# Optimization experiments

Measured on AMD Instinct MI355X. Metric: run time of the kernel, lower is better.

Reference implementation:

```python
import jax, jax.numpy as jnp
import numpy as np

HEADS = 16
LN_EPS = 1e-5


def setup_inputs() -> dict:
    key = jax.random.key(0)
    ks = jax.random.split(key, 8)
    B, S, D = 2, 2048, 1024
    F = 4 * D
    std = 0.02
    return {
        "x": jax.random.normal(ks[0], (B, S, D), jnp.float32),
        # QKV projections (stored as (in, out)); kaiming-normal-like scale
        "Wq": jax.random.normal(ks[1], (D, D), jnp.float32) * std,
        "bq": jnp.zeros((D,), jnp.float32),
        "Wk": jax.random.normal(ks[2], (D, D), jnp.float32) * std,
        "bk": jnp.zeros((D,), jnp.float32),
        "Wv": jax.random.normal(ks[3], (D, D), jnp.float32) * std,
        "bv": jnp.zeros((D,), jnp.float32),
        # FFN
        "W1": jax.random.normal(ks[4], (D, F), jnp.float32) * std,
        "b1": jnp.zeros((F,), jnp.float32),
        "W2": jax.random.normal(ks[5], (F, D), jnp.float32) * std,
        "b2": jnp.zeros((D,), jnp.float32),
        # LayerNorm
        "gamma": jnp.ones((D,), jnp.float32),
        "beta": jnp.zeros((D,), jnp.float32),
    }


def reference(x, Wq, bq, Wk, bk, Wv, bv, W1, b1, W2, b2, gamma, beta):
    B, S, D = x.shape
    H = HEADS
    hd = D // H
    # QKV projections -> [B, H, S, hd]
    Q = (x @ Wq + bq).reshape(B, S, H, hd).transpose(0, 2, 1, 3)
    K = (x @ Wk + bk).reshape(B, S, H, hd).transpose(0, 2, 1, 3)
    V = (x @ Wv + bv).reshape(B, S, H, hd).transpose(0, 2, 1, 3)
    # scores scaled by sqrt(embedding_dim), faithful to source (not head_dim)
    scores = jnp.einsum('bhqd,bhkd->bhqk', Q, K) / jnp.sqrt(jnp.asarray(D, x.dtype))
    attn = jax.nn.softmax(scores, axis=-1)
    # diagonal_training: zero the diagonal of the post-softmax attention matrix
    attn = attn * (1.0 - jnp.eye(S, dtype=attn.dtype))
    out = jnp.einsum('bhqk,bhkd->bhqd', attn, V)
    out = out.transpose(0, 2, 1, 3).reshape(B, S, D)
    # dropout is identity in eval mode
    h = jax.nn.gelu(out @ W1 + b1, approximate=False) @ W2 + b2
    # LayerNorm
    mu = jnp.mean(h, axis=-1, keepdims=True)
    var = jnp.var(h, axis=-1, keepdims=True)
    return (h - mu) * jax.lax.rsqrt(var + LN_EPS) * gamma + beta
```

## Files before the change

### kernel.cpp

```cpp
#include <hip/hip_runtime.h>

using bf16x8 = __attribute__((ext_vector_type(8))) short;
using f32x4  = __attribute__((ext_vector_type(4))) float;

__device__ __forceinline__ float b2f(ushort u) {
  union { unsigned int i; float f; } v; v.i = ((unsigned int)u) << 16; return v.f;
}
__device__ __forceinline__ ushort f2b(float f) {
  unsigned int x = __float_as_uint(f);
  unsigned int r = (x + 0x7FFFu + ((x >> 16) & 1u)) >> 16;
  return (ushort)r;
}
__device__ __forceinline__ unsigned cvt_pk_bf16(float a, float b) {
  unsigned r;
  asm("v_cvt_pk_bf16_f32 %0, %1, %2" : "=v"(r) : "v"(a), "v"(b));
  return r;
}

__device__ __forceinline__ void gld_lds16(const void* g, void* l) {
  __builtin_amdgcn_global_load_lds(
      (const __attribute__((address_space(1))) void*)g,
      (__attribute__((address_space(3))) void*)l, 16, 0, 0);
}


__global__ void cast_bf16_kernel(const float* __restrict__ in, ushort* __restrict__ out, int n) {
  int i = (blockIdx.x * blockDim.x + threadIdx.x) * 4;
  if (i < n) {
    float4 v = *(const float4*)(in + i);
    ushort4 o = make_ushort4(f2b(v.x), f2b(v.y), f2b(v.z), f2b(v.w));
    *(ushort4*)(out + i) = o;
  }
}

__global__ void transpose_cast_kernel(const float* __restrict__ in, ushort* __restrict__ out,
                                      int R, int C) {
  __shared__ float tile[32][33];
  int tx = threadIdx.x, ty = threadIdx.y;
  int cb = blockIdx.x * 32, rb = blockIdx.y * 32;
  for (int i = ty; i < 32; i += 8)
    tile[i][tx] = in[(size_t)(rb + i) * C + (cb + tx)];
  __syncthreads();
  for (int i = ty; i < 32; i += 8)
    out[(size_t)(cb + i) * R + (rb + tx)] = f2b(tile[tx][i]);
}

__global__ void transpose_cast_qkv_kernel(const float* __restrict__ Wq,
                                          const float* __restrict__ Wk,
                                          const float* __restrict__ Wv,
                                          ushort* __restrict__ out) {
  __shared__ float tile[32][33];
  const float* in = (blockIdx.z == 0) ? Wq : (blockIdx.z == 1) ? Wk : Wv;
  ushort* dst = out + (size_t)blockIdx.z * 1024 * 1024;
  int tx = threadIdx.x, ty = threadIdx.y;
  int cb = blockIdx.x * 32, rb = blockIdx.y * 32;
  for (int i = ty; i < 32; i += 8)
    tile[i][tx] = in[(size_t)(rb + i) * 1024 + (cb + tx)];
  __syncthreads();
  for (int i = ty; i < 32; i += 8)
    dst[(size_t)(cb + i) * 1024 + (rb + tx)] = f2b(tile[tx][i]);
}

__global__ void transpose_v_kernel(const ushort* __restrict__ V, ushort* __restrict__ Vt) {
  __shared__ ushort t[32][33];
  int bh = blockIdx.z;
  int b = bh >> 4, h = bh & 15;
  int s0 = blockIdx.x * 32, d0 = blockIdx.y * 32;
  const ushort* Vbp = V + ((size_t)b * 2048) * 1024 + h * 64;
  ushort* Vtb = Vt + (size_t)bh * 64 * 2048;
  int tx = threadIdx.x, ty = threadIdx.y;
  for (int i = ty; i < 32; i += 8) t[i][tx] = Vbp[(size_t)(s0 + i) * 1024 + d0 + tx];
  __syncthreads();
  for (int i = ty; i < 32; i += 8) Vtb[(size_t)(d0 + i) * 2048 + s0 + tx] = t[tx][i];
}


template<int EPI>
__global__ __launch_bounds__(512) void gemm256(
    const ushort* __restrict__ A, const ushort* __restrict__ Bt,
    const float* __restrict__ bias, void* __restrict__ Cout,
    int M, int N, int K)
{
  extern __shared__ ushort lds[];

  const int nwg = gridDim.x * gridDim.y;
  const int bid = blockIdx.y * gridDim.x + blockIdx.x;
  const int cpx = nwg >> 3;
  const int swz = (bid & 7) * cpx + (bid >> 3);
  const int bm = (swz % gridDim.x) * 256;
  const int bn = (swz / gridDim.x) * 256;

  const int tid = threadIdx.x;
  const int lane = tid & 63, w = tid >> 6;
  const int wr = w >> 2, wc = w & 3;
  const int hi = lane >> 4, c = lane & 15;

  const int srow0 = tid >> 3;
  const int scolx = (((tid & 7) ^ (srow0 & 7)) * 8);
  const ushort* gA = A  + (size_t)(bm + srow0) * K + scolx;
  const ushort* gB = Bt + (size_t)(bn + srow0) * K + scolx;

  const int NT = K / 64;
  f32x4 acc[8][4] = {};

  auto STAGE = [&](int buf, int t) {
    ushort* bA = lds + buf * 32768;
    ushort* bB = bA + 16384;
    const size_t ko = (size_t)t * 64;
    #pragma unroll
    for (int ch = 0; ch < 4; ++ch) {
      gld_lds16(gA + (size_t)ch * 64 * K + ko, bA + ch * 4096 + tid * 8);
      gld_lds16(gB + (size_t)ch * 64 * K + ko, bB + ch * 4096 + tid * 8);
    }
  };

  STAGE(0, 0);
  __syncthreads();

  int cur = 0;
  for (int t = 0; t < NT; ++t) {
    if (t + 1 < NT) STAGE(cur ^ 1, t + 1);
    const ushort* sA = lds + cur * 32768;
    const ushort* sB = sA + 16384;
    #pragma unroll
    for (int kk = 0; kk < 2; ++kk) {
      bf16x8 bf[4], af[8];
      #pragma unroll
      for (int n = 0; n < 4; ++n) {
        int row = wc * 64 + n * 16 + c;
        bf[n] = *(const bf16x8*)&sB[row * 64 + (((kk * 4 + hi) ^ (c & 7)) * 8)];
      }
      #pragma unroll
      for (int m = 0; m < 8; ++m) {
        int row = wr * 128 + m * 16 + c;
        af[m] = *(const bf16x8*)&sA[row * 64 + (((kk * 4 + hi) ^ (c & 7)) * 8)];
      }
      __builtin_amdgcn_s_setprio(1);
      #pragma unroll
      for (int m = 0; m < 8; ++m)
        #pragma unroll
        for (int n = 0; n < 4; ++n)
          acc[m][n] = __builtin_amdgcn_mfma_f32_16x16x32_bf16(af[m], bf[n], acc[m][n], 0, 0, 0);
      __builtin_amdgcn_s_setprio(0);
    }
    __syncthreads();
    cur ^= 1;
  }

  ushort* eb = &lds[w * 1088];
  const int g = hi;
  const int er = lane >> 3;
  const int es = (lane & 7) * 8;
  float bia[4];
  #pragma unroll
  for (int n = 0; n < 4; ++n) bia[n] = bias[bn + wc * 64 + n * 16 + c];

  #pragma unroll
  for (int mf = 0; mf < 8; ++mf) {
    #pragma unroll
    for (int n = 0; n < 4; ++n) {
      #pragma unroll
      for (int r = 0; r < 4; ++r) {
        float v = acc[mf][n][r] + bia[n];
        if (EPI == 1) {
          float u = 0.7978845608028654f * (v + 0.044715f * v * v * v);
          float au = fabsf(u);
          float e = __expf(-2.0f * au);
          float th = (1.0f - e) / (1.0f + e);
          th = copysignf(th, u);
          v = 0.5f * v * (1.0f + th);
        }
        eb[(g * 4 + r) * 68 + n * 16 + c] = f2b(v);
      }
    }
    asm volatile("" ::: "memory");
    bf16x8 v0 = *(const bf16x8*)&eb[er * 68 + es];
    bf16x8 v1 = *(const bf16x8*)&eb[(er + 8) * 68 + es];
    int grow = bm + wr * 128 + mf * 16 + er;
    int gcol = bn + wc * 64 + es;
    if (EPI == 3) {
      ushort* dst = (ushort*)Cout + (size_t)(gcol >> 10) * 4194304 + (gcol & 1023);
      *(bf16x8*)(dst + (size_t)grow * 1024) = v0;
      *(bf16x8*)(dst + (size_t)(grow + 8) * 1024) = v1;
    } else {
      ushort* dst = (ushort*)Cout + gcol;
      *(bf16x8*)(dst + (size_t)grow * N) = v0;
      *(bf16x8*)(dst + (size_t)(grow + 8) * N) = v1;
    }
    asm volatile("" ::: "memory");
  }
}


#define BM 128
#define BN 128
#define BK 32

__global__ __launch_bounds__(256) void gemm_bf16_f32(
    const ushort* __restrict__ A, const ushort* __restrict__ Bt,
    float* __restrict__ C0, float* __restrict__ C1,
    float* __restrict__ C2, float* __restrict__ C3,
    int M, int N, int Kstride, int k_len)
{
  __shared__ ushort Asm_[2][BM * BK];
  __shared__ ushort Bsm_[2][BN * BK];
  const int bm = blockIdx.x * BM, bn = blockIdx.y * BN;
  const int k_begin = blockIdx.z * k_len;
  const int tid = threadIdx.x;
  const int lane = tid & 63, w = tid >> 6;
  const int wm = (w >> 1) * 64, wn = (w & 1) * 64;
  const int g = lane >> 4, c = lane & 15;
  const int swz8 = ((g ^ ((c >> 1) & 3)) * 8);
  const int srow = tid >> 2;
  const int scol = (((tid & 3) ^ ((srow >> 1) & 3)) * 8);
  const int soff = srow * 32 + (tid & 3) * 8;

  const ushort* gA0 = A  + (size_t)(bm + srow) * Kstride + k_begin + scol;
  const ushort* gA1 = gA0 + (size_t)64 * Kstride;
  const ushort* gB0 = Bt + (size_t)(bn + srow) * Kstride + k_begin + scol;
  const ushort* gB1 = gB0 + (size_t)64 * Kstride;

  f32x4 acc[4][4] = {};
  const int nt = k_len / BK;

  gld_lds16(gA0, &Asm_[0][soff]);
  gld_lds16(gA1, &Asm_[0][64 * 32 + soff]);
  gld_lds16(gB0, &Bsm_[0][soff]);
  gld_lds16(gB1, &Bsm_[0][64 * 32 + soff]);
  __syncthreads();

  int cur = 0;
  for (int t = 0; t < nt; ++t) {
    if (t + 1 < nt) {
      int k0 = (t + 1) * BK;
      gld_lds16(gA0 + k0, &Asm_[cur ^ 1][soff]);
      gld_lds16(gA1 + k0, &Asm_[cur ^ 1][64 * 32 + soff]);
      gld_lds16(gB0 + k0, &Bsm_[cur ^ 1][soff]);
      gld_lds16(gB1 + k0, &Bsm_[cur ^ 1][64 * 32 + soff]);
    }
    bf16x8 af[4], bfr[4];
    #pragma unroll
    for (int m = 0; m < 4; ++m)
      af[m] = *(const bf16x8*)&Asm_[cur][(wm + m * 16 + c) * 32 + swz8];
    #pragma unroll
    for (int n = 0; n < 4; ++n)
      bfr[n] = *(const bf16x8*)&Bsm_[cur][(wn + n * 16 + c) * 32 + swz8];
    #pragma unroll
    for (int m = 0; m < 4; ++m)
      #pragma unroll
      for (int n = 0; n < 4; ++n)
        acc[m][n] = __builtin_amdgcn_mfma_f32_16x16x32_bf16(af[m], bfr[n], acc[m][n], 0, 0, 0);
    __syncthreads();
    cur ^= 1;
  }

  float* dst = C0;
  if (blockIdx.z == 1) dst = C1;
  else if (blockIdx.z == 2) dst = C2;
  else if (blockIdx.z == 3) dst = C3;

  #pragma unroll
  for (int n = 0; n < 4; ++n) {
    int col = bn + wn + n * 16 + c;
    #pragma unroll
    for (int m = 0; m < 4; ++m)
      #pragma unroll
      for (int r = 0; r < 4; ++r) {
        int row = bm + wm + m * 16 + g * 4 + r;
        dst[(size_t)row * N + col] = acc[m][n][r];
      }
  }
}


#define ATT_SC2 0.0450842202f

__global__ __launch_bounds__(512) void attn_kernel(
    const ushort* __restrict__ Q, const ushort* __restrict__ K,
    const ushort* __restrict__ V, const ushort* __restrict__ Vt,
    ushort* __restrict__ Out)
{
  const int bid = blockIdx.x;
  const int tile = (bid & 7) * 64 + (bid >> 3);
  const int bh = tile >> 4;
  const int q0 = (tile & 15) * 128;
  const int b = bh >> 4, h = bh & 15;
  const int tid = threadIdx.x;
  const int w = tid >> 6, lane = tid & 63;
  const int hi = lane >> 4, c = lane & 15;
  const int qw = q0 + w * 16;

  const size_t boff = ((size_t)b * 2048) * 1024 + h * 64;
  const ushort* Qp = Q + boff;
  const ushort* Kp = K + boff;
  const ushort* Vp = V + boff;
  const ushort* Vtb = Vt + (size_t)bh * 64 * 2048;

  __shared__ ushort Ksm[2][64 * 64];
  __shared__ ushort Vsm[2][64 * 64];
  __shared__ ushort Psm[8][16 * 72];

  const int srow = tid >> 3;
  const int sslot = tid & 7;
  const int scolx = ((sslot ^ (srow & 7)) * 8);
  const ushort* gK = Kp + (size_t)srow * 1024 + scolx;
  const ushort* gV = Vtb + (size_t)srow * 2048 + scolx;

  bf16x8 qf0 = *(const bf16x8*)(Qp + (size_t)(qw + c) * 1024 + hi * 8);
  bf16x8 qf1 = *(const bf16x8*)(Qp + (size_t)(qw + c) * 1024 + 32 + hi * 8);
  {
    ushort* q0p = (ushort*)&qf0;
    ushort* q1p = (ushort*)&qf1;
    #pragma unroll
    for (int j = 0; j < 8; ++j) {
      q0p[j] = f2b(b2f(q0p[j]) * ATT_SC2);
      q1p[j] = f2b(b2f(q1p[j]) * ATT_SC2);
    }
  }

  f32x4 acc[4] = {};
  float l_run = 0.f;

  gld_lds16(gK, &Ksm[0][tid * 8]);
  gld_lds16(gV, &Vsm[0][tid * 8]);
  __syncthreads();

  const int nt = 2048 / 64;
  for (int t = 0; t < nt; ++t) {
    const int buf = t & 1;
    if (t + 1 < nt) {
      gld_lds16(gK + (size_t)(t + 1) * 64 * 1024, &Ksm[buf ^ 1][tid * 8]);
      gld_lds16(gV + (size_t)(t + 1) * 64,        &Vsm[buf ^ 1][tid * 8]);
    }

    f32x4 sv[4];
    __builtin_amdgcn_s_setprio(1);
    #pragma unroll
    for (int sub = 0; sub < 4; ++sub) {
      int rr = sub * 16 + c;
      int sw = (rr & 7) * 8;
      bf16x8 k0 = *(const bf16x8*)&Ksm[buf][rr * 64 + ((hi * 8) ^ sw)];
      bf16x8 k1 = *(const bf16x8*)&Ksm[buf][rr * 64 + ((32 + hi * 8) ^ sw)];
      f32x4 z = {};
      z = __builtin_amdgcn_mfma_f32_16x16x32_bf16(k0, qf0, z, 0, 0, 0);
      z = __builtin_amdgcn_mfma_f32_16x16x32_bf16(k1, qf1, z, 0, 0, 0);
      sv[sub] = z;
    }
    __builtin_amdgcn_s_setprio(0);

    float p[16];
    float psum = 0.f;
    #pragma unroll
    for (int sub = 0; sub < 4; ++sub)
      #pragma unroll
      for (int r = 0; r < 4; ++r) { float e = exp2f(sv[sub][r]); p[sub * 4 + r] = e; psum += e; }
    psum += __shfl_xor(psum, 16);
    psum += __shfl_xor(psum, 32);
    l_run += psum;

    #pragma unroll
    for (int sub = 0; sub < 4; ++sub) {
      uint2 pk;
      pk.x = cvt_pk_bf16(p[sub * 4 + 0], p[sub * 4 + 1]);
      pk.y = cvt_pk_bf16(p[sub * 4 + 2], p[sub * 4 + 3]);
      *(uint2*)&Psm[w][c * 72 + sub * 16 + hi * 4] = pk;
    }
    asm volatile("" ::: "memory");

    bf16x8 pa0 = *(const bf16x8*)&Psm[w][c * 72 + hi * 8];
    bf16x8 pa1 = *(const bf16x8*)&Psm[w][c * 72 + 32 + hi * 8];
    __builtin_amdgcn_s_setprio(1);
    #pragma unroll
    for (int dsub = 0; dsub < 4; ++dsub) {
      int rr = dsub * 16 + c;
      int sw = (rr & 7) * 8;
      bf16x8 v0 = *(const bf16x8*)&Vsm[buf][rr * 64 + ((hi * 8) ^ sw)];
      bf16x8 v1 = *(const bf16x8*)&Vsm[buf][rr * 64 + ((32 + hi * 8) ^ sw)];
      acc[dsub] = __builtin_amdgcn_mfma_f32_16x16x32_bf16(pa0, v0, acc[dsub], 0, 0, 0);
      acc[dsub] = __builtin_amdgcn_mfma_f32_16x16x32_bf16(pa1, v1, acc[dsub], 0, 0, 0);
    }
    __builtin_amdgcn_s_setprio(0);

    __syncthreads();
  }

  #pragma unroll
  for (int r = 0; r < 4; ++r) {
    int q = qw + hi * 4 + r;
    float part = 0.f;
    #pragma unroll
    for (int t = 0; t < 4; ++t)
      part += b2f(Qp[(size_t)q * 1024 + c * 4 + t]) * b2f(Kp[(size_t)q * 1024 + c * 4 + t]);
    #pragma unroll
    for (int off = 1; off < 16; off <<= 1) part += __shfl_xor(part, off);
    float lq = __shfl(l_run, hi * 4 + r, 16);
    float pqq = exp2f(part * ATT_SC2);
    float inv = 1.f / lq;
    #pragma unroll
    for (int dsub = 0; dsub < 4; ++dsub) {
      float vq = b2f(Vp[(size_t)q * 1024 + dsub * 16 + c]);
      float o = (acc[dsub][r] - pqq * vq) * inv;
      Out[((size_t)(b * 2048 + q) * 16 + h) * 64 + dsub * 16 + c] = f2b(o);
    }
  }
}


__global__ __launch_bounds__(256) void ln_kernel(float* __restrict__ h,
                                                 const float* __restrict__ p1,
                                                 const float* __restrict__ p2,
                                                 const float* __restrict__ p3,
                                                 const float* __restrict__ b2,
                                                 const float* __restrict__ gamma,
                                                 const float* __restrict__ beta, int np) {
  int row = blockIdx.x, tid = threadIdx.x;
  float* hr = h + (size_t)row * 1024;
  float4 v = ((const float4*)hr)[tid];
  float4 p = ((const float4*)(p1 + (size_t)row * 1024))[tid];
  float4 bb = ((const float4*)b2)[tid];
  v.x += p.x + bb.x; v.y += p.y + bb.y; v.z += p.z + bb.z; v.w += p.w + bb.w;
  if (np == 4) {
    float4 a = ((const float4*)(p2 + (size_t)row * 1024))[tid];
    float4 d = ((const float4*)(p3 + (size_t)row * 1024))[tid];
    v.x += a.x + d.x; v.y += a.y + d.y; v.z += a.z + d.z; v.w += a.w + d.w;
  }
  float s = v.x + v.y + v.z + v.w;
  #pragma unroll
  for (int off = 1; off < 64; off <<= 1) s += __shfl_xor(s, off);
  __shared__ float red[2][4];
  int wv = tid >> 6, lane = tid & 63;
  if (lane == 0) red[0][wv] = s;
  __syncthreads();
  float mu = (red[0][0] + red[0][1] + red[0][2] + red[0][3]) * (1.0f / 1024.0f);
  float dx = v.x - mu, dy = v.y - mu, dz = v.z - mu, dw = v.w - mu;
  float q = dx * dx + dy * dy + dz * dz + dw * dw;
  #pragma unroll
  for (int off = 1; off < 64; off <<= 1) q += __shfl_xor(q, off);
  if (lane == 0) red[1][wv] = q;
  __syncthreads();
  float var = (red[1][0] + red[1][1] + red[1][2] + red[1][3]) * (1.0f / 1024.0f);
  float is = rsqrtf(var + 1e-5f);
  float4 gm = ((const float4*)gamma)[tid];
  float4 bt = ((const float4*)beta)[tid];
  float4 o;
  o.x = dx * is * gm.x + bt.x;
  o.y = dy * is * gm.y + bt.y;
  o.z = dz * is * gm.z + bt.z;
  o.w = dw * is * gm.w + bt.w;
  ((float4*)hr)[tid] = o;
}


extern "C" void kernel_launch(void* const* d_in, const int* in_sizes, int n_in,
                              void* d_out, int out_size, void* d_ws, size_t ws_size,
                              hipStream_t stream) {
  const float* x  = (const float*)d_in[0];
  const float* Wq = (const float*)d_in[1];
  const float* bq = (const float*)d_in[2];
  const float* Wk = (const float*)d_in[3];
  const float* bk = (const float*)d_in[4];
  const float* Wv = (const float*)d_in[5];
  const float* bv = (const float*)d_in[6];
  const float* W1 = (const float*)d_in[7];
  const float* b1 = (const float*)d_in[8];
  const float* W2 = (const float*)d_in[9];
  const float* b2 = (const float*)d_in[10];
  const float* gamma = (const float*)d_in[11];
  const float* beta  = (const float*)d_in[12];
  float* out = (float*)d_out;

  char* ws = (char*)d_ws;
  const size_t MB = 1u << 20;
  ushort* xb    = (ushort*)(ws + 0);
  ushort* Wqkvt = (ushort*)(ws + 8 * MB);
  ushort* Qb    = (ushort*)(ws + 14 * MB);
  ushort* Kb    = (ushort*)(ws + 22 * MB);
  ushort* Vb    = (ushort*)(ws + 30 * MB);
  ushort* Vt    = (ushort*)(ws + 38 * MB);
  ushort* AO    = (ushort*)(ws + 46 * MB);
  ushort* W1t   = (ushort*)(ws + 54 * MB);
  ushort* h1    = (ushort*)(ws + 0);
  ushort* W2t   = (ushort*)(ws + 32 * MB);
  float*  p1    = (float*)(ws + 40 * MB);
  float*  p2    = (float*)(ws + 56 * MB);
  float*  p3    = (float*)(ws + 72 * MB);
  float*  bqkv  = (float*)(ws + 46 * MB);

  const bool split4 = (ws_size >= (size_t)89 * MB);

  (void)hipMemcpyAsync(bqkv,        bq, 4096, hipMemcpyDeviceToDevice, stream);
  (void)hipMemcpyAsync(bqkv + 1024, bk, 4096, hipMemcpyDeviceToDevice, stream);
  (void)hipMemcpyAsync(bqkv + 2048, bv, 4096, hipMemcpyDeviceToDevice, stream);

  dim3 tb(32, 8);
  cast_bf16_kernel<<<4096, 256, 0, stream>>>(x, xb, 4194304);
  transpose_cast_qkv_kernel<<<dim3(32, 32, 3), tb, 0, stream>>>(Wq, Wk, Wv, Wqkvt);
  transpose_cast_kernel<<<dim3(128, 32), tb, 0, stream>>>(W1, W1t, 1024, 4096);

  gemm256<3><<<dim3(16, 12), 512, 131072, stream>>>(xb, Wqkvt, bqkv, Qb, 4096, 3072, 1024);

  transpose_v_kernel<<<dim3(64, 2, 32), tb, 0, stream>>>(Vb, Vt);

  attn_kernel<<<512, 512, 0, stream>>>(Qb, Kb, Vb, Vt, AO);

  transpose_cast_kernel<<<dim3(32, 128), tb, 0, stream>>>(W2, W2t, 4096, 1024);

  gemm256<1><<<dim3(16, 16), 512, 131072, stream>>>(AO, W1t, b1, h1, 4096, 4096, 1024);

  if (split4) {
    gemm_bf16_f32<<<dim3(32, 8, 4), 256, 0, stream>>>(h1, W2t, out, p1, p2, p3,
                                                      4096, 1024, 4096, 1024);
    ln_kernel<<<4096, 256, 0, stream>>>(out, p1, p2, p3, b2, gamma, beta, 4);
  } else {
    gemm_bf16_f32<<<dim3(32, 8, 2), 256, 0, stream>>>(h1, W2t, out, p1, nullptr, nullptr,
                                                      4096, 1024, 4096, 2048);
    ln_kernel<<<4096, 256, 0, stream>>>(out, p1, nullptr, nullptr, b2, gamma, beta, 2);
  }
}
```

Before: 237.3 us.

## Restructure GEMM main loop into fine-grained 8-phase ping-pong pipeline

Replaces the double-buffered GEMM mainloop with a schedule of eight phases per pair of K-tiles. Each K-half (32 wide) of A and B is staged separately with a new swizzle, and global-to-LDS loads are interleaved into individual MFMA phases with explicit vmcnt waits and s_barrier pairs. The goal is to overlap memory traffic with MFMA work more finely and to lower register pressure by holding only 4 A fragments at a time. In exchange it adds many more barriers per tile, which can cost throughput, and it assumes NT is even.

```diff
diff --git a/kernel.cpp b/kernel.cpp
--- a/kernel.cpp
+++ b/kernel.cpp
@@ -75,13 +75,49 @@
 }
 
 
+#define FENCE asm volatile("" ::: "memory")
+#define VM10  asm volatile("s_waitcnt vmcnt(10)" ::: "memory")
+#define VM0   asm volatile("s_waitcnt vmcnt(0)" ::: "memory")
+
+#define STAGE_A(kt, kk) do {                                                   \
+    ushort* d_ = ldsm + ((kt) & 1) * 16384 + (kk) * 8192 + tid * 8;            \
+    const ushort* s_ = gAs + (kt) * 64 + (kk) * 32;                            \
+    gld_lds16(s_, d_); gld_lds16(s_ + rowK128, d_ + 4096); } while (0)
+#define STAGE_B(kt, kk) do {                                                   \
+    ushort* d_ = ldsm + 32768 + ((kt) & 1) * 16384 + (kk) * 8192 + tid * 8;    \
+    const ushort* s_ = gBs + (kt) * 64 + (kk) * 32;                            \
+    gld_lds16(s_, d_); gld_lds16(s_ + rowK128, d_ + 4096); } while (0)
+
+#define PHASE(kt, kk, mq, STAGE_STMT, WAIT_STMT)                               \
+  {                                                                            \
+    FENCE;                                                                     \
+    const ushort* hA = ldsm + ((kt) & 1) * 16384 + (kk) * 8192;                \
+    if ((mq) == 0) {                                                           \
+      const ushort* hB = ldsm + 32768 + ((kt) & 1) * 16384 + (kk) * 8192;      \
+      _Pragma("unroll") for (int n_ = 0; n_ < 4; ++n_)                         \
+        bf[n_] = *(const bf16x8*)&hB[(wc * 64 + n_ * 16 + c) * 32 + bsw];      \
+    }                                                                          \
+    _Pragma("unroll") for (int m_ = 0; m_ < 4; ++m_)                           \
+      af[m_] = *(const bf16x8*)&hA[(wr * 128 + (mq) * 64 + m_ * 16 + c) * 32 + bsw]; \
+    STAGE_STMT;                                                                \
+    WAIT_STMT;                                                                 \
+    __builtin_amdgcn_s_barrier();                                              \
+    __builtin_amdgcn_s_setprio(1);                                             \
+    _Pragma("unroll") for (int m_ = 0; m_ < 4; ++m_)                           \
+      _Pragma("unroll") for (int n_ = 0; n_ < 4; ++n_)                         \
+        acc[(mq) * 4 + m_][n_] = __builtin_amdgcn_mfma_f32_16x16x32_bf16(      \
+            af[m_], bf[n_], acc[(mq) * 4 + m_][n_], 0, 0, 0);                  \
+    __builtin_amdgcn_s_setprio(0);                                             \
+    __builtin_amdgcn_s_barrier();                                              \
+  }
+
 template<int EPI>
 __global__ __launch_bounds__(512) void gemm256(
     const ushort* __restrict__ A, const ushort* __restrict__ Bt,
     const float* __restrict__ bias, void* __restrict__ Cout,
     int M, int N, int K)
 {
-  extern __shared__ ushort lds[];
+  extern __shared__ ushort ldsm[];
 
   const int nwg = gridDim.x * gridDim.y;
   const int bid = blockIdx.y * gridDim.x + blockIdx.x;
@@ -94,60 +130,51 @@
   const int lane = tid & 63, w = tid >> 6;
   const int wr = w >> 2, wc = w & 3;
   const int hi = lane >> 4, c = lane & 15;
-
-  const int srow0 = tid >> 3;
-  const int scolx = (((tid & 7) ^ (srow0 & 7)) * 8);
-  const ushort* gA = A  + (size_t)(bm + srow0) * K + scolx;
-  const ushort* gB = Bt + (size_t)(bn + srow0) * K + scolx;
-
-  const int NT = K / 64;
+  const int bsw = (hi ^ ((c >> 1) & 3)) * 8;
+
+  const int str = tid >> 2;
+  const int stc = ((tid & 3) ^ ((tid >> 3) & 3)) * 8;
+  const ushort* gAs = A  + (size_t)(bm + str) * K + stc;
+  const ushort* gBs = Bt + (size_t)(bn + str) * K + stc;
+  const size_t rowK128 = (size_t)128 * K;
+
+  const int NTt = K / 64;
+  const int NI = NTt / 2;
+
   f32x4 acc[8][4] = {};
-
-  auto STAGE = [&](int buf, int t) {
-    ushort* bA = lds + buf * 32768;
-    ushort* bB = bA + 16384;
-    const size_t ko = (size_t)t * 64;
-    #pragma unroll
-    for (int ch = 0; ch < 4; ++ch) {
-      gld_lds16(gA + (size_t)ch * 64 * K + ko, bA + ch * 4096 + tid * 8);
-      gld_lds16(gB + (size_t)ch * 64 * K + ko, bB + ch * 4096 + tid * 8);
-    }
-  };
-
-  STAGE(0, 0);
-  __syncthreads();
-
-  int cur = 0;
-  for (int t = 0; t < NT; ++t) {
-    if (t + 1 < NT) STAGE(cur ^ 1, t + 1);
-    const ushort* sA = lds + cur * 32768;
-    const ushort* sB = sA + 16384;
-    #pragma unroll
-    for (int kk = 0; kk < 2; ++kk) {
-      bf16x8 bf[4], af[8];
-      #pragma unroll
-      for (int n = 0; n < 4; ++n) {
-        int row = wc * 64 + n * 16 + c;
-        bf[n] = *(const bf16x8*)&sB[row * 64 + (((kk * 4 + hi) ^ (c & 7)) * 8)];
-      }
-      #pragma unroll
-      for (int m = 0; m < 8; ++m) {
-        int row = wr * 128 + m * 16 + c;
-        af[m] = *(const bf16x8*)&sA[row * 64 + (((kk * 4 + hi) ^ (c & 7)) * 8)];
-      }
-      __builtin_amdgcn_s_setprio(1);
-      #pragma unroll
-      for (int m = 0; m < 8; ++m)
-        #pragma unroll
-        for (int n = 0; n < 4; ++n)
-          acc[m][n] = __builtin_amdgcn_mfma_f32_16x16x32_bf16(af[m], bf[n], acc[m][n], 0, 0, 0);
-      __builtin_amdgcn_s_setprio(0);
-    }
-    __syncthreads();
-    cur ^= 1;
-  }
-
-  ushort* eb = &lds[w * 1088];
+  bf16x8 af[4], bf[4];
+
+  STAGE_B(0, 0); STAGE_A(0, 0); STAGE_B(0, 1); STAGE_A(0, 1);
+  STAGE_B(1, 0); STAGE_A(1, 0); STAGE_B(1, 1);
+  asm volatile("s_waitcnt vmcnt(6)" ::: "memory");
+  __builtin_amdgcn_s_barrier();
+
+  for (int j = 0; j < NI; ++j) {
+    const int e = 2 * j, o = e + 1;
+    if (j + 1 < NI) {
+      PHASE(e, 0, 0, STAGE_A(o, 1),     (void)0);
+      PHASE(e, 0, 1, STAGE_B(e + 2, 0), VM10);
+      PHASE(e, 1, 0, STAGE_A(e + 2, 0), (void)0);
+      PHASE(e, 1, 1, STAGE_B(e + 2, 1), VM10);
+      PHASE(o, 0, 0, STAGE_A(e + 2, 1), (void)0);
+      PHASE(o, 0, 1, STAGE_B(o + 2, 0), VM10);
+      PHASE(o, 1, 0, STAGE_A(o + 2, 0), (void)0);
+      PHASE(o, 1, 1, STAGE_B(o + 2, 1), VM10);
+    } else {
+      PHASE(e, 0, 0, STAGE_A(o, 1), (void)0);
+      PHASE(e, 0, 1, (void)0,       VM0);
+      PHASE(e, 1, 0, (void)0,       (void)0);
+      PHASE(e, 1, 1, (void)0,       VM0);
+      PHASE(o, 0, 0, (void)0,       (void)0);
+      PHASE(o, 0, 1, (void)0,       VM0);
+      PHASE(o, 1, 0, (void)0,       (void)0);
+      PHASE(o, 1, 1, (void)0,       (void)0);
+    }
+  }
+
+  __syncthreads();
+
+  ushort* eb = &ldsm[w * 1088];
   const int g = hi;
   const int er = lane >> 3;
   const int es = (lane & 7) * 8;
```

After: 379.3 us. +59.9%, slower.
